# Performance work log

Measured on AMD Instinct MI355X. Metric: run time of the kernel, lower is better.

Reference implementation:

```python
import jax, jax.numpy as jnp
import numpy as np

NB = 4
QN = -(2 ** (NB - 1))   # -8
QP = 2 ** (NB - 1) - 1  # 7
EPS = 1e-5


def _grad_scale(x, g):
    # forward: x, backward: grad * g (LSQ gradient scaling)
    return x * g + jax.lax.stop_gradient(x - x * g)


def _round_pass(x):
    # round with straight-through estimator
    return x + jax.lax.stop_gradient(jnp.round(x) - x)


def _lsq(v, alpha, qn, qp):
    # LSQ fake quantize-dequantize with learnable step size alpha
    g = 1.0 / np.sqrt(v.size * qp)
    a = _grad_scale(alpha, g)
    return _round_pass(jnp.clip(v / a, qn, qp)) * a


def _bn(x, g, b, m, v):
    # eval-mode BatchNorm2d over channel dim of NCHW
    s = (g * jax.lax.rsqrt(v + EPS))[None, :, None, None]
    return (x - m[None, :, None, None]) * s + b[None, :, None, None]


def _conv(x, w, stride, pad, groups):
    return jax.lax.conv_general_dilated(
        x, w, (stride, stride), pad,
        dimension_numbers=('NCHW', 'OIHW', 'NCHW'),
        feature_group_count=groups)


def setup_inputs() -> dict:
    key = jax.random.key(0)
    ks = jax.random.split(key, 4)
    inp, oup, hid = 96, 96, 576
    B, H, W = 32, 28, 28
    d = {}
    d['x'] = jax.random.normal(ks[0], (B, inp, H, W), jnp.float32)
    d['w1'] = jax.random.normal(ks[1], (hid, inp, 1, 1), jnp.float32) * 0.1
    d['w2'] = jax.random.normal(ks[2], (hid, 1, 3, 3), jnp.float32) * 0.1
    d['w3'] = jax.random.normal(ks[3], (oup, hid, 1, 1), jnp.float32) * 0.1
    for i, c in zip((1, 2, 3), (hid, hid, oup)):
        d[f'aw{i}'] = jnp.full((1,), 0.05, jnp.float32)  # weight step size
        d[f'ax{i}'] = jnp.full((1,), 0.5, jnp.float32)   # activation step size
        d[f'g{i}'] = jnp.ones((c,), jnp.float32)
        d[f'b{i}'] = jnp.zeros((c,), jnp.float32)
        d[f'm{i}'] = jnp.zeros((c,), jnp.float32)
        d[f'v{i}'] = jnp.ones((c,), jnp.float32)
    return d


def reference(x, w1, w2, w3, aw1, ax1, g1, b1, m1, v1,
              aw2, ax2, g2, b2, m2, v2, aw3, ax3, g3, b3, m3, v3):
    hid = w1.shape[0]
    # 1x1 expand conv (LSQ on activation and weight)
    h = _conv(_lsq(x, ax1, QN, QP), _lsq(w1, aw1, QN, QP), 1, [(0, 0), (0, 0)], 1)
    h = jnp.clip(_bn(h, g1, b1, m1, v1), 0.0, 6.0)
    # 3x3 depthwise conv, stride 1
    h = _conv(_lsq(h, ax2, QN, QP), _lsq(w2, aw2, QN, QP), 1, [(1, 1), (1, 1)], hid)
    h = jnp.clip(_bn(h, g2, b2, m2, v2), 0.0, 6.0)
    # 1x1 project conv
    h = _conv(_lsq(h, ax3, QN, QP), _lsq(w3, aw3, QN, QP), 1, [(0, 0), (0, 0)], 1)
    h = _bn(h, g3, b3, m3, v3)
    # identity residual (stride==1 and inp==oup)
    return x + h
```

## Files before the change

### kernel.cpp

```cpp
#include <hip/hip_runtime.h>

#define EPSF 1e-5f
#define MAGICF 12582912.0f
#define MLO 0x4B3FFFF8
#define MHI 0x4B400007

typedef int    int4v   __attribute__((ext_vector_type(4)));
typedef float  float4v __attribute__((ext_vector_type(4)));

#define W1P_OFF  0
#define W3P_OFF  55296
#define W2T_OFF  110592
#define S1B1_OFF 119808
#define S2B2_OFF 124416
#define S3B3_OFF 129024

#define H1S 296
#define H2S 304

__device__ __forceinline__ float lsq_q(float v, float a) {
    float t = v / a;
    t = fminf(fmaxf(t, -8.0f), 7.0f);
    return rintf(t);
}

__device__ __forceinline__ long q8pack_w(const float* w, int base, const int* idx, float a) {
    unsigned long long v = 0;
    #pragma unroll
    for (int j = 0; j < 8; ++j) {
        int q = (int)lsq_q(w[base + idx[j]], a);
        v |= (unsigned long long)(q & 255) << (8 * j);
    }
    return (long)v;
}

__global__ __launch_bounds__(128)
void prep_w(const float* __restrict__ w1, const float* __restrict__ w2,
            const float* __restrict__ w3,
            const float* aw1, const float* ax1, const float* ax2,
            const float* aw2, const float* ax3, const float* aw3,
            const float* __restrict__ g1, const float* __restrict__ b1,
            const float* __restrict__ m1, const float* __restrict__ v1,
            const float* __restrict__ g2, const float* __restrict__ b2,
            const float* __restrict__ m2, const float* __restrict__ v2,
            const float* __restrict__ g3, const float* __restrict__ b3,
            const float* __restrict__ m3, const float* __restrict__ v3,
            long* __restrict__ w1p, long* __restrict__ w3p,
            int* __restrict__ w2t,
            float* __restrict__ s1b1, float* __restrict__ s2b2,
            float* __restrict__ s3b3) {
    int id = blockIdx.x * 128 + threadIdx.x;
    const int lin[8] = {0, 1, 2, 3, 4, 5, 6, 7};
    const int prm[8] = {0, 2, 4, 6, 1, 3, 5, 7};
    if (id < 6912) {
        int l = id & 63, t = id >> 6;
        int kc = t % 3, ct = t / 3;
        int co = ct * 16 + (l & 15);
        int ci0 = kc * 32 + (l >> 4) * 8;
        w1p[id] = q8pack_w(w1, co * 96 + ci0, lin, aw1[0]);
    } else if (id < 13824) {
        int i = id - 6912;
        int l = i & 63, t = i >> 6;
        int kc = t % 18, ct = t / 18;
        int co = ct * 16 + (l & 15);
        int ci0 = kc * 32 + (l >> 4) * 8;
        w3p[i] = q8pack_w(w3, co * 576 + ci0, prm, aw3[0]);
    } else if (id < 14400) {
        int ch = id - 13824;
        int q[9];
        #pragma unroll
        for (int tp = 0; tp < 9; ++tp)
            q[tp] = (int)lsq_q(w2[ch * 9 + tp], aw2[0]) & 255;
        w2t[ch * 4 + 0] = q[0] | (q[1] << 8) | (q[2] << 16) | (q[3] << 24);
        w2t[ch * 4 + 1] = q[4] | (q[5] << 8) | (q[6] << 16) | (q[7] << 24);
        w2t[ch * 4 + 2] = q[8];
        w2t[ch * 4 + 3] = 0;
    } else if (id < 14976) {
        int c = id - 14400;
        float s = g1[c] / sqrtf(v1[c] + EPSF);
        float A = aw1[0] * ax1[0];
        float inv = 1.0f / ax2[0];
        s1b1[c] = A * s * inv;
        s1b1[576 + c] = (b1[c] - m1[c] * s) * inv;
    } else if (id < 15552) {
        int c = id - 14976;
        float s = g2[c] / sqrtf(v2[c] + EPSF);
        float A = ax2[0] * aw2[0];
        float inv = 1.0f / ax3[0];
        s2b2[c] = A * s * inv;
        s2b2[576 + c] = (b2[c] - m2[c] * s) * inv;
    } else if (id < 15648) {
        int c = id - 15552;
        float s = g3[c] / sqrtf(v3[c] + EPSF);
        float A = ax3[0] * aw3[0];
        s3b3[c] = A * s;
        s3b3[96 + c] = b3[c] - m3[c] * s;
    }
}

__global__ __launch_bounds__(448, 4)
void fused_k(const float* __restrict__ x, const long* __restrict__ w1p,
             const int* __restrict__ w2tg, const long* __restrict__ w3p,
             const float* __restrict__ ax1,
             const float* __restrict__ s1b1g, const float* __restrict__ s2b2g,
             const float* __restrict__ s3b3g, float* __restrict__ out) {
    __shared__ __align__(16) signed char h1[120 * H1S];
    __shared__ __align__(16) signed char h2[64 * H2S];
    __shared__ __align__(16) float l1[1152];
    __shared__ __align__(16) float l2[1152];
    __shared__ __align__(16) float l3[192];
    __shared__ __align__(16) int4v l2t[576];
    const int tid = threadIdx.x;
    const int w = tid >> 6, l = tid & 63;
    const int quad = l >> 4, c16 = l & 15;
    const int qh = quad >> 1, ql = quad & 1;
    const int b = blockIdx.x;
    const int r0 = blockIdx.y * 2;

    {
        const int lp = w * 16 + c16;
        const int row = lp / 28, col = lp - (lp / 28) * 28;
        const int img_row = r0 - 1 + row;
        const bool valid = (unsigned)img_row < 28u;
        const int p = min(max(img_row, 0), 27) * 28 + col;
        const float inv1 = 1.0f / ax1[0];

        float xv[3][8];
        #pragma unroll
        for (int kc = 0; kc < 3; ++kc) {
            const float* xs = x + (b * 96 + kc * 32 + quad * 8) * 784 + p;
            #pragma unroll
            for (int j = 0; j < 8; ++j) xv[kc][j] = xs[j * 784];
        }

        for (int i = tid; i < 120 * H1S / 16; i += 448)
            ((int4v*)h1)[i] = (int4v){0, 0, 0, 0};
        if (tid < 288) {
            ((int4v*)l1)[tid] = ((const int4v*)s1b1g)[tid];
            ((int4v*)l2)[tid] = ((const int4v*)s2b2g)[tid];
        }
        if (tid < 48) ((int4v*)l3)[tid] = ((const int4v*)s3b3g)[tid];
        for (int i = tid; i < 576; i += 448) l2t[i] = ((const int4v*)w2tg)[i];
        __syncthreads();

        long bfr[3];
        #pragma unroll
        for (int kc = 0; kc < 3; ++kc) {
            unsigned long long v = 0;
            #pragma unroll
            for (int j = 0; j < 8; ++j) {
                int qi = __float_as_int(fmaf(xv[kc][j], inv1, MAGICF));
                qi = min(max(qi, MLO), MHI);
                v |= (unsigned long long)(qi & 255) << (8 * j);
            }
            bfr[kc] = (long)v;
        }
        const int pos_h = row * 30 + col + 1;
        #pragma unroll 4
        for (int ct = 0; ct < 36; ++ct) {
            int4v acc; acc[0] = 0; acc[1] = 0; acc[2] = 0; acc[3] = 0;
            #pragma unroll
            for (int kc = 0; kc < 3; ++kc)
                acc = __builtin_amdgcn_mfma_i32_16x16x32_i8(
                    w1p[(ct * 3 + kc) * 64 + l], bfr[kc], acc, 0, 0, 0);
            const int co0 = ct * 16 + quad * 4;
            float4v S = *(const float4v*)(l1 + co0);
            float4v B = *(const float4v*)(l1 + 576 + co0);
            int pk = 0;
            #pragma unroll
            for (int r2 = 0; r2 < 4; ++r2) {
                float t = fmaf((float)acc[r2], S[r2], B[r2]);
                t = __builtin_amdgcn_fmed3f(t, 0.0f, 7.0f);
                pk |= (__float_as_int(t + MAGICF) & 15) << (4 * r2);
            }
            if (valid)
                *(unsigned short*)(h1 + pos_h * H1S + (co0 >> 1)) = (unsigned short)pk;
        }
    }
    __syncthreads();

    {
        const bool vald = ((c16 >> 3) == ql);
        const int mh = c16 & 7;
        const int jj = (mh >> 1) | ((mh & 1) << 2);
        const unsigned shla = 8u * (jj & 3);
        const unsigned mlo = (jj < 4) ? 0xFFFFFFFFu : 0u;
        const unsigned mhi = ~mlo;
        const unsigned vm  = vald ? 0xFFu : 0u;
        const unsigned vm4 = (vald && qh == 0) ? 0xFFu : 0u;
        const unsigned sh0 = qh * 8u;
        const unsigned sh1 = 16u + qh * 8u;

        #pragma unroll 2
        for (int t = w; t < 144; t += 7) {
            const int pt = t / 36, ct = t - (t / 36) * 36;
            const int pos = pt * 16 + c16;
            const int posc = min(pos, 55);
            const int row_in = posc / 28, col = posc - (posc / 28) * 28;
            const int choff = ct * 8 + ql * 4;
            const int4v tw = l2t[ct * 16 + c16];
            int4v acc; acc[0] = 0; acc[1] = 0; acc[2] = 0; acc[3] = 0;
            #pragma unroll
            for (int kc = 0; kc < 5; ++kc) {
                unsigned bb;
                if      (kc == 0) bb = ((unsigned)tw[0] >> sh0) & vm;
                else if (kc == 1) bb = ((unsigned)tw[0] >> sh1) & vm;
                else if (kc == 2) bb = ((unsigned)tw[1] >> sh0) & vm;
                else if (kc == 3) bb = ((unsigned)tw[1] >> sh1) & vm;
                else              bb = ((unsigned)tw[2]) & vm4;
                const unsigned pl = bb << shla;
                const long afrag = (long)(((unsigned long long)(pl & mhi) << 32)
                                          | (pl & mlo));
                const int tap = min(kc * 2 + qh, 8);
                const int dh = tap / 3 - 1, dc = tap - (tap / 3) * 3 - 1;
                const int pos_h = (row_in + 1 + dh) * 30 + (col + 1 + dc);
                const unsigned v = *(const unsigned*)(h1 + pos_h * H1S + choff);
                const unsigned lo = v & 0x0F0F0F0Fu;
                const unsigned hi = (v >> 4) & 0x0F0F0F0Fu;
                acc = __builtin_amdgcn_mfma_i32_16x16x32_i8(
                    afrag, (long)(((unsigned long long)hi << 32) | lo), acc, 0, 0, 0);
            }
            if (pos < 56) {
                const int c0 = ct * 16 + quad * 4;
                float4v S = *(const float4v*)(l2 + c0);
                float4v B = *(const float4v*)(l2 + 576 + c0);
                int pk = 0;
                #pragma unroll
                for (int r2 = 0; r2 < 4; ++r2) {
                    float tt = fmaf((float)acc[r2], S[r2], B[r2]);
                    tt = __builtin_amdgcn_fmed3f(tt, 0.0f, 7.0f);
                    pk |= (__float_as_int(tt + MAGICF) & 15) << (4 * r2);
                }
                *(unsigned short*)(h2 + pos * H2S + (c0 >> 1)) = (unsigned short)pk;
            }
        }
    }
    __syncthreads();

    #pragma unroll 2
    for (int t = w; t < 24; t += 7) {
        const int nt = t / 6, ct = t - (t / 6) * 6;
        const int nloc = nt * 16 + quad * 4;
        const int co = ct * 16 + c16;
        const int off = (b * 96 + co) * 784 + r0 * 28 + min(nloc, 52);
        const float4v xr = *(const float4v*)(x + off);
        const float S = l3[co], Bv = l3[96 + co];
        int4v acc; acc[0] = 0; acc[1] = 0; acc[2] = 0; acc[3] = 0;
        const signed char* arow = h2 + (nt * 16 + c16) * H2S + quad * 4;
        #pragma unroll 6
        for (int kc = 0; kc < 18; ++kc) {
            const unsigned va = *(const unsigned*)(arow + kc * 16);
            const unsigned lo = va & 0x0F0F0F0Fu;
            const unsigned hi = (va >> 4) & 0x0F0F0F0Fu;
            acc = __builtin_amdgcn_mfma_i32_16x16x32_i8(
                (long)(((unsigned long long)hi << 32) | lo),
                w3p[(ct * 18 + kc) * 64 + l], acc, 0, 0, 0);
        }
        if (nloc < 56) {
            float4v o;
            #pragma unroll
            for (int r2 = 0; r2 < 4; ++r2)
                o[r2] = fmaf((float)acc[r2], S, Bv) + xr[r2];
            *(float4v*)(out + off) = o;
        }
    }
}

extern "C" void kernel_launch(void* const* d_in, const int* in_sizes, int n_in,
                              void* d_out, int out_size, void* d_ws, size_t ws_size,
                              hipStream_t stream) {
    const float* x   = (const float*)d_in[0];
    const float* w1  = (const float*)d_in[1];
    const float* w2  = (const float*)d_in[2];
    const float* w3  = (const float*)d_in[3];
    const float* aw1 = (const float*)d_in[4];
    const float* ax1 = (const float*)d_in[5];
    const float* g1  = (const float*)d_in[6];
    const float* b1  = (const float*)d_in[7];
    const float* m1  = (const float*)d_in[8];
    const float* v1  = (const float*)d_in[9];
    const float* aw2 = (const float*)d_in[10];
    const float* ax2 = (const float*)d_in[11];
    const float* g2  = (const float*)d_in[12];
    const float* b2  = (const float*)d_in[13];
    const float* m2  = (const float*)d_in[14];
    const float* v2  = (const float*)d_in[15];
    const float* aw3 = (const float*)d_in[16];
    const float* ax3 = (const float*)d_in[17];
    const float* g3  = (const float*)d_in[18];
    const float* b3  = (const float*)d_in[19];
    const float* m3  = (const float*)d_in[20];
    const float* v3  = (const float*)d_in[21];

    char* ws = (char*)d_ws;
    long* w1p = (long*)(ws + W1P_OFF);
    long* w3p = (long*)(ws + W3P_OFF);
    int*  w2t = (int*)(ws + W2T_OFF);
    float* s1b1 = (float*)(ws + S1B1_OFF);
    float* s2b2 = (float*)(ws + S2B2_OFF);
    float* s3b3 = (float*)(ws + S3B3_OFF);

    float* out = (float*)d_out;

    prep_w<<<123, 128, 0, stream>>>(w1, w2, w3, aw1, ax1, ax2, aw2, ax3, aw3,
                                    g1, b1, m1, v1, g2, b2, m2, v2, g3, b3, m3, v3,
                                    w1p, w3p, w2t, s1b1, s2b2, s3b3);
    dim3 grid(32, 14);
    fused_k<<<grid, 448, 0, stream>>>(x, w1p, w2t, w3p, ax1, s1b1, s2b2, s3b3, out);
}
```

Baseline: 139.0 us.

## Split fused block into expand-conv kernel and depthwise+project kernel via global buffer

Splits the single fused kernel into two kernels. The first computes the 1x1 expand conv and writes the 4-bit packed activations to a global workspace buffer of about 7 MB. The second loads a 3-row halo from that buffer, then runs the depthwise 3x3 and project conv one output row per block. This removes the halo recompute of conv1 rows (each 2-row block previously computed 4 input rows) and raises block count. The cost is a global round-trip for the intermediate, an extra launch, and a fallback to the old path when the workspace is too small.

```diff
diff --git a/kernel.cpp b/kernel.cpp
--- a/kernel.cpp
+++ b/kernel.cpp
@@ -14,9 +14,12 @@
 #define S1B1_OFF 119808
 #define S2B2_OFF 124416
 #define S3B3_OFF 129024
-
-#define H1S 296
+#define H1G_OFF  130048
+#define H1G_NEED (130048u + 32u * 28u * 28u * 288u)
+
+#define H1S 304
 #define H2S 304
+#define F1S 296
 
 __device__ __forceinline__ float lsq_q(float v, float a) {
     float t = v / a;
@@ -98,13 +101,187 @@
     }
 }
 
+
+__global__ __launch_bounds__(512, 4)
+void conv1_k(const float* __restrict__ x, const long* __restrict__ w1p,
+             const float* __restrict__ ax1, const float* __restrict__ s1b1,
+             signed char* __restrict__ h1g) {
+    const int tid = threadIdx.x;
+    const int w = tid >> 6, l = tid & 63;
+    const int quad = l >> 4, c16 = l & 15;
+    const int tile = w >> 2, ctg = (w & 3) * 9;
+    const int b = blockIdx.x, r = blockIdx.y;
+    const int pos = tile == 0 ? c16 : 12 + c16;
+    const int p = r * 28 + pos;
+    const float inv1 = 1.0f / ax1[0];
+
+    long bfr[3];
+    #pragma unroll
+    for (int kc = 0; kc < 3; ++kc) {
+        const float* xs = x + (b * 96 + kc * 32 + quad * 8) * 784 + p;
+        unsigned long long v = 0;
+        #pragma unroll
+        for (int j = 0; j < 8; ++j) {
+            int qi = __float_as_int(fmaf(xs[j * 784], inv1, MAGICF));
+            qi = min(max(qi, MLO), MHI);
+            v |= (unsigned long long)(qi & 255) << (8 * j);
+        }
+        bfr[kc] = (long)v;
+    }
+    signed char* orow = h1g + ((b * 28 + r) * 28 + pos) * 288;
+    const bool dostore = (tile == 0) | (c16 >= 4);
+    #pragma unroll
+    for (int ci = 0; ci < 9; ++ci) {
+        const int ct = ctg + ci;
+        int4v acc; acc[0] = 0; acc[1] = 0; acc[2] = 0; acc[3] = 0;
+        #pragma unroll
+        for (int kc = 0; kc < 3; ++kc)
+            acc = __builtin_amdgcn_mfma_i32_16x16x32_i8(
+                w1p[(ct * 3 + kc) * 64 + l], bfr[kc], acc, 0, 0, 0);
+        const int co0 = ct * 16 + quad * 4;
+        float4v S = *(const float4v*)(s1b1 + co0);
+        float4v B = *(const float4v*)(s1b1 + 576 + co0);
+        int pk = 0;
+        #pragma unroll
+        for (int r2 = 0; r2 < 4; ++r2) {
+            float t = fmaf((float)acc[r2], S[r2], B[r2]);
+            t = __builtin_amdgcn_fmed3f(t, 0.0f, 7.0f);
+            pk |= (__float_as_int(t + MAGICF) & 15) << (4 * r2);
+        }
+        if (dostore)
+            *(unsigned short*)(orow + (co0 >> 1)) = (unsigned short)pk;
+    }
+}
+
+__global__ __launch_bounds__(384, 4)
+void dwc3_k(const float* __restrict__ x, const signed char* __restrict__ h1g,
+            const int* __restrict__ w2tg, const long* __restrict__ w3p,
+            const float* __restrict__ s2b2g, const float* __restrict__ s3b3g,
+            float* __restrict__ out) {
+    __shared__ __align__(16) signed char h1[90 * H1S];
+    __shared__ __align__(16) signed char h2[32 * H2S];
+    __shared__ __align__(16) float l2[1152];
+    __shared__ __align__(16) float l3[192];
+    __shared__ __align__(16) int4v l2t[576];
+    const int tid = threadIdx.x;
+    const int w = tid >> 6, l = tid & 63;
+    const int quad = l >> 4, c16 = l & 15;
+    const int qh = quad >> 1, ql = quad & 1;
+    const int b = blockIdx.x;
+    const int r = blockIdx.y;
+
+    if (tid < 288) ((int4v*)l2)[tid] = ((const int4v*)s2b2g)[tid];
+    if (tid < 48)  ((int4v*)l3)[tid] = ((const int4v*)s3b3g)[tid];
+    for (int i = tid; i < 576; i += 384) l2t[i] = ((const int4v*)w2tg)[i];
+    for (int idx = tid; idx < 3024; idx += 384) {
+        const int hr = idx / 1008, rem = idx - hr * 1008;
+        const int pc = rem / 36, k = rem - pc * 36;
+        const int ir = r - 1 + hr;
+        long val = 0;
+        if ((unsigned)ir < 28u)
+            val = *(const long*)(h1g + ((b * 28 + ir) * 28 + pc) * 288 + k * 8);
+        *(long*)(h1 + (hr * 30 + pc + 1) * H1S + k * 8) = val;
+    }
+    for (int idx = tid; idx < 216; idx += 384) {
+        const int hr = idx / 72, rem = idx - hr * 72;
+        const int c = rem / 36, k = rem - c * 36;
+        *(long*)(h1 + (hr * 30 + (c ? 29 : 0)) * H1S + k * 8) = 0;
+    }
+    __syncthreads();
+
+    {
+        const bool vald = ((c16 >> 3) == ql);
+        const int mh = c16 & 7;
+        const int jj = (mh >> 1) | ((mh & 1) << 2);
+        const unsigned shla = 8u * (jj & 3);
+        const unsigned mlo = (jj < 4) ? 0xFFFFFFFFu : 0u;
+        const unsigned mhi = ~mlo;
+        const unsigned vm  = vald ? 0xFFu : 0u;
+        const unsigned vm4 = (vald && qh == 0) ? 0xFFu : 0u;
+        const unsigned sh0 = qh * 8u;
+        const unsigned sh1 = 16u + qh * 8u;
+
+        #pragma unroll 2
+        for (int t = w; t < 72; t += 6) {
+            const int pt = t / 36, ct = t - (t / 36) * 36;
+            const int pos = pt * 16 + c16;
+            const int col = min(pos, 27);
+            const int choff = ct * 8 + ql * 4;
+            const int4v tw = l2t[ct * 16 + c16];
+            int4v acc; acc[0] = 0; acc[1] = 0; acc[2] = 0; acc[3] = 0;
+            #pragma unroll
+            for (int kc = 0; kc < 5; ++kc) {
+                unsigned bb;
+                if      (kc == 0) bb = ((unsigned)tw[0] >> sh0) & vm;
+                else if (kc == 1) bb = ((unsigned)tw[0] >> sh1) & vm;
+                else if (kc == 2) bb = ((unsigned)tw[1] >> sh0) & vm;
+                else if (kc == 3) bb = ((unsigned)tw[1] >> sh1) & vm;
+                else              bb = ((unsigned)tw[2]) & vm4;
+                const unsigned pl = bb << shla;
+                const long afrag = (long)(((unsigned long long)(pl & mhi) << 32)
+                                          | (pl & mlo));
+                const int tap = min(kc * 2 + qh, 8);
+                const int dh = tap / 3 - 1, dc = tap - (tap / 3) * 3 - 1;
+                const int pos_h = (1 + dh) * 30 + (col + 1 + dc);
+                const unsigned v = *(const unsigned*)(h1 + pos_h * H1S + choff);
+                const unsigned lo = v & 0x0F0F0F0Fu;
+                const unsigned hi = (v >> 4) & 0x0F0F0F0Fu;
+                acc = __builtin_amdgcn_mfma_i32_16x16x32_i8(
+                    afrag, (long)(((unsigned long long)hi << 32) | lo), acc, 0, 0, 0);
+            }
+            if (pos < 28) {
+                const int c0 = ct * 16 + quad * 4;
+                float4v S = *(const float4v*)(l2 + c0);
+                float4v B = *(const float4v*)(l2 + 576 + c0);
+                int pk = 0;
+                #pragma unroll
+                for (int r2 = 0; r2 < 4; ++r2) {
+                    float tt = fmaf((float)acc[r2], S[r2], B[r2]);
+                    tt = __builtin_amdgcn_fmed3f(tt, 0.0f, 7.0f);
+                    pk |= (__float_as_int(tt + MAGICF) & 15) << (4 * r2);
+                }
+                *(unsigned short*)(h2 + pos * H2S + (c0 >> 1)) = (unsigned short)pk;
+            }
+        }
+    }
+    __syncthreads();
+
+    #pragma unroll 2
+    for (int t = w; t < 12; t += 6) {
+        const int nt = t / 6, ct = t - (t / 6) * 6;
+        const int nloc = nt * 16 + quad * 4;
+        const int co = ct * 16 + c16;
+        const int off = (b * 96 + co) * 784 + r * 28 + min(nloc, 24);
+        const float4v xr = *(const float4v*)(x + off);
+        const float S = l3[co], Bv = l3[96 + co];
+        int4v acc; acc[0] = 0; acc[1] = 0; acc[2] = 0; acc[3] = 0;
+        const signed char* arow = h2 + (nt * 16 + c16) * H2S + quad * 4;
+        #pragma unroll 6
+        for (int kc = 0; kc < 18; ++kc) {
+            const unsigned va = *(const unsigned*)(arow + kc * 16);
+            const unsigned lo = va & 0x0F0F0F0Fu;
+            const unsigned hi = (va >> 4) & 0x0F0F0F0Fu;
+            acc = __builtin_amdgcn_mfma_i32_16x16x32_i8(
+                (long)(((unsigned long long)hi << 32) | lo),
+                w3p[(ct * 18 + kc) * 64 + l], acc, 0, 0, 0);
+        }
+        if (nloc < 28) {
+            float4v o;
+            #pragma unroll
+            for (int r2 = 0; r2 < 4; ++r2)
+                o[r2] = fmaf((float)acc[r2], S, Bv) + xr[r2];
+            *(float4v*)(out + off) = o;
+        }
+    }
+}
+
 __global__ __launch_bounds__(448, 4)
 void fused_k(const float* __restrict__ x, const long* __restrict__ w1p,
              const int* __restrict__ w2tg, const long* __restrict__ w3p,
              const float* __restrict__ ax1,
              const float* __restrict__ s1b1g, const float* __restrict__ s2b2g,
              const float* __restrict__ s3b3g, float* __restrict__ out) {
-    __shared__ __align__(16) signed char h1[120 * H1S];
+    __shared__ __align__(16) signed char h1[120 * F1S];
     __shared__ __align__(16) signed char h2[64 * H2S];
     __shared__ __align__(16) float l1[1152];
     __shared__ __align__(16) float l2[1152];
@@ -132,8 +309,7 @@
             #pragma unroll
             for (int j = 0; j < 8; ++j) xv[kc][j] = xs[j * 784];
         }
-
-        for (int i = tid; i < 120 * H1S / 16; i += 448)
+        for (int i = tid; i < 120 * F1S / 16; i += 448)
             ((int4v*)h1)[i] = (int4v){0, 0, 0, 0};
         if (tid < 288) {
             ((int4v*)l1)[tid] = ((const int4v*)s1b1g)[tid];
@@ -174,7 +350,7 @@
                 pk |= (__float_as_int(t + MAGICF) & 15) << (4 * r2);
             }
             if (valid)
-                *(unsigned short*)(h1 + pos_h * H1S + (co0 >> 1)) = (unsigned short)pk;
+                *(unsigned short*)(h1 + pos_h * F1S + (co0 >> 1)) = (unsigned short)pk;
         }
     }
     __syncthreads();
@@ -214,7 +390,7 @@
                 const int tap = min(kc * 2 + qh, 8);
                 const int dh = tap / 3 - 1, dc = tap - (tap / 3) * 3 - 1;
                 const int pos_h = (row_in + 1 + dh) * 30 + (col + 1 + dc);
-                const unsigned v = *(const unsigned*)(h1 + pos_h * H1S + choff);
+                const unsigned v = *(const unsigned*)(h1 + pos_h * F1S + choff);
                 const unsigned lo = v & 0x0F0F0F0Fu;
                 const unsigned hi = (v >> 4) & 0x0F0F0F0Fu;
                 acc = __builtin_amdgcn_mfma_i32_16x16x32_i8(
@@ -305,6 +481,14 @@
     prep_w<<<123, 128, 0, stream>>>(w1, w2, w3, aw1, ax1, ax2, aw2, ax3, aw3,
                                     g1, b1, m1, v1, g2, b2, m2, v2, g3, b3, m3, v3,
                                     w1p, w3p, w2t, s1b1, s2b2, s3b3);
-    dim3 grid(32, 14);
-    fused_k<<<grid, 448, 0, stream>>>(x, w1p, w2t, w3p, ax1, s1b1, s2b2, s3b3, out);
-}
+
+    if (ws_size >= (size_t)H1G_NEED) {
+        signed char* h1g = (signed char*)(ws + H1G_OFF);
+        dim3 grid(32, 28);
+        conv1_k<<<grid, 512, 0, stream>>>(x, w1p, ax1, s1b1, h1g);
+        dwc3_k<<<grid, 384, 0, stream>>>(x, h1g, w2t, w3p, s2b2, s3b3, out);
+    } else {
+        dim3 grid(32, 14);
+        fused_k<<<grid, 448, 0, stream>>>(x, w1p, w2t, w3p, ax1, s1b1, s2b2, s3b3, out);
+    }
+}
```

Measured after the change: 153.1 us. 10.2% more time.

## Stage expand-conv weights through double-buffered LDS reusing h2 buffer

Applied to the files above, without the earlier changes.

Stage-1 expand weights are no longer read per-wave from global memory. They are cooperatively loaded into an LDS double buffer carved out of the unused h2 scratch. The next chunk is prefetched into registers while the current chunk's MFMAs run. This cuts redundant global/L2 weight traffic across the block's waves, at the cost of six extra block barriers and LDS store/load traffic.

```diff
diff --git a/kernel.cpp b/kernel.cpp
--- a/kernel.cpp
+++ b/kernel.cpp
@@ -15,7 +15,7 @@
 #define S2B2_OFF 124416
 #define S3B3_OFF 129024
 
-#define H1S 296
+#define F1S 296
 #define H2S 304
 
 __device__ __forceinline__ float lsq_q(float v, float a) {
@@ -104,7 +104,7 @@
              const float* __restrict__ ax1,
              const float* __restrict__ s1b1g, const float* __restrict__ s2b2g,
              const float* __restrict__ s3b3g, float* __restrict__ out) {
-    __shared__ __align__(16) signed char h1[120 * H1S];
+    __shared__ __align__(16) signed char h1[120 * F1S];
     __shared__ __align__(16) signed char h2[64 * H2S];
     __shared__ __align__(16) float l1[1152];
     __shared__ __align__(16) float l2[1152];
@@ -133,7 +133,8 @@
             for (int j = 0; j < 8; ++j) xv[kc][j] = xs[j * 784];
         }
 
-        for (int i = tid; i < 120 * H1S / 16; i += 448)
+        long* wstage = (long*)h2;
+        for (int i = tid; i < 120 * F1S / 16; i += 448)
             ((int4v*)h1)[i] = (int4v){0, 0, 0, 0};
         if (tid < 288) {
             ((int4v*)l1)[tid] = ((const int4v*)s1b1g)[tid];
@@ -141,6 +142,7 @@
         }
         if (tid < 48) ((int4v*)l3)[tid] = ((const int4v*)s3b3g)[tid];
         for (int i = tid; i < 576; i += 448) l2t[i] = ((const int4v*)w2tg)[i];
+        for (int i = tid; i < 1152; i += 448) wstage[i] = w1p[i];
         __syncthreads();
 
         long bfr[3];
@@ -156,28 +158,46 @@
             bfr[kc] = (long)v;
         }
         const int pos_h = row * 30 + col + 1;
-        #pragma unroll 4
-        for (int ct = 0; ct < 36; ++ct) {
-            int4v acc; acc[0] = 0; acc[1] = 0; acc[2] = 0; acc[3] = 0;
-            #pragma unroll
-            for (int kc = 0; kc < 3; ++kc)
-                acc = __builtin_amdgcn_mfma_i32_16x16x32_i8(
-                    w1p[(ct * 3 + kc) * 64 + l], bfr[kc], acc, 0, 0, 0);
-            const int co0 = ct * 16 + quad * 4;
-            float4v S = *(const float4v*)(l1 + co0);
-            float4v B = *(const float4v*)(l1 + 576 + co0);
-            int pk = 0;
-            #pragma unroll
-            for (int r2 = 0; r2 < 4; ++r2) {
-                float t = fmaf((float)acc[r2], S[r2], B[r2]);
-                t = __builtin_amdgcn_fmed3f(t, 0.0f, 7.0f);
-                pk |= (__float_as_int(t + MAGICF) & 15) << (4 * r2);
-            }
-            if (valid)
-                *(unsigned short*)(h1 + pos_h * H1S + (co0 >> 1)) = (unsigned short)pk;
-        }
-    }
-    __syncthreads();
+
+        for (int c = 0; c < 6; ++c) {
+            long st0 = 0, st1 = 0, st2 = 0;
+            if (c < 5) {
+                const long* src = w1p + (c + 1) * 1152;
+                st0 = src[tid];
+                st1 = src[tid + 448];
+                if (tid < 256) st2 = src[tid + 896];
+            }
+            const long* cur = wstage + (c & 1) * 1152;
+            #pragma unroll 3
+            for (int ctl = 0; ctl < 6; ++ctl) {
+                const int ct = c * 6 + ctl;
+                int4v acc; acc[0] = 0; acc[1] = 0; acc[2] = 0; acc[3] = 0;
+                #pragma unroll
+                for (int kc = 0; kc < 3; ++kc)
+                    acc = __builtin_amdgcn_mfma_i32_16x16x32_i8(
+                        cur[(ctl * 3 + kc) * 64 + l], bfr[kc], acc, 0, 0, 0);
+                const int co0 = ct * 16 + quad * 4;
+                float4v S = *(const float4v*)(l1 + co0);
+                float4v B = *(const float4v*)(l1 + 576 + co0);
+                int pk = 0;
+                #pragma unroll
+                for (int r2 = 0; r2 < 4; ++r2) {
+                    float t = fmaf((float)acc[r2], S[r2], B[r2]);
+                    t = __builtin_amdgcn_fmed3f(t, 0.0f, 7.0f);
+                    pk |= (__float_as_int(t + MAGICF) & 15) << (4 * r2);
+                }
+                if (valid)
+                    *(unsigned short*)(h1 + pos_h * F1S + (co0 >> 1)) = (unsigned short)pk;
+            }
+            if (c < 5) {
+                long* dst = wstage + ((c + 1) & 1) * 1152;
+                dst[tid] = st0;
+                dst[tid + 448] = st1;
+                if (tid < 256) dst[tid + 896] = st2;
+            }
+            __syncthreads();
+        }
+    }
 
     {
         const bool vald = ((c16 >> 3) == ql);
@@ -214,7 +234,7 @@
                 const int tap = min(kc * 2 + qh, 8);
                 const int dh = tap / 3 - 1, dc = tap - (tap / 3) * 3 - 1;
                 const int pos_h = (row_in + 1 + dh) * 30 + (col + 1 + dc);
-                const unsigned v = *(const unsigned*)(h1 + pos_h * H1S + choff);
+                const unsigned v = *(const unsigned*)(h1 + pos_h * F1S + choff);
                 const unsigned lo = v & 0x0F0F0F0Fu;
                 const unsigned hi = (v >> 4) & 0x0F0F0F0Fu;
                 acc = __builtin_amdgcn_mfma_i32_16x16x32_i8(
```

Measured after the change: 136.2 us. -2.0%, faster.
